# Kernel tuning notes

Measured on AMD Instinct MI355X. Metric: run time of the kernel, lower is better.

## Reference

```python
import jax, jax.numpy as jnp
import numpy as np

RE_PER_PRB = 12  # resource elements (subcarriers) per PRB in 5G NR


def _forward(y, h_hat_ls, dmrs_ofdm_pos, dmrs_subcarrier_pos):
    S = y.shape[2]  # num_ofdm_symbols (y used for its shape only)
    # [B, num_pilots, T, R] -> [B, R, T, num_pilots]
    h = jnp.transpose(h_hat_ls, (0, 3, 2, 1))
    B, R, T, P = h.shape
    # FOCC removal: average adjacent pilot pairs, duplicate back (sum/2, repeat 2)
    h = h.reshape(B, R, T, P // 2, 2).sum(axis=-1, keepdims=True) * 0.5
    h = jnp.broadcast_to(h, (B, R, T, P // 2, 2)).reshape(B, R, T, P)

    npd = dmrs_subcarrier_pos.shape[1]   # pilots per DMRS symbol per PRB
    nds = dmrs_ofdm_pos.shape[-1]        # number of DMRS OFDM symbols
    nprb = P // (npd * nds)              # number of PRBs
    RE = RE_PER_PRB

    # --- nearest-pilot indices + positional encodings, per tx (as in torch code,
    # torch.meshgrid default indexing='ij') ---
    re_pos = jnp.stack(
        jnp.meshgrid(jnp.arange(RE), jnp.arange(S), indexing='ij'), axis=-1
    ).reshape(-1, 1, 2)  # [RE*S, 1, 2]

    def per_tx(sc_pos, of_pos):
        pil = jnp.stack(jnp.meshgrid(sc_pos, of_pos, indexing='ij'), axis=-1).reshape(1, -1, 2)
        diff = jnp.abs(re_pos - pil)                  # [RE*S, npd*nds, 2] Manhattan components
        nn = jnp.argmin(diff.sum(-1), axis=1).reshape(S, RE)
        pe = diff.min(axis=1).reshape(S, RE, 2).transpose(1, 0, 2).astype(jnp.float32)  # [RE, S, 2]
        norm = lambda x: (x - x.mean()) / (x.std(ddof=1) + 1e-8)  # torch .std() is unbiased
        # channel order swapped exactly as in the torch code: [time-dist, freq-dist]
        return nn, jnp.stack([norm(pe[..., 1]), norm(pe[..., 0])], axis=-1)

    nn_idx, pe = jax.vmap(per_tx)(dmrs_subcarrier_pos, dmrs_ofdm_pos)  # [T,S,RE], [T,RE,S,2]
    pe = jnp.tile(pe, (1, nprb, 1, 1))  # [T, nprb*RE, S, 2]

    # --- group pilots per PRB ---
    # pilot layout in h_hat_ls: (dmrs_symbol, prb, subcarrier); per-PRB pilot index
    # = subcarrier*nds + symbol to match the meshgrid('ij') flattening above
    hp = h.reshape(B, R, T, nds, nprb, npd).transpose(0, 1, 2, 4, 5, 3)
    hp = hp.reshape(B, R, T, nprb, npd * nds)  # [B,R,T,nprb,pilots_per_prb]

    # --- nearest-neighbor gather onto the full resource grid ---
    gather_tx = lambda hp_t, nn_t: hp_t[..., nn_t]  # [B,R,nprb,Np] , [S,RE] -> [B,R,nprb,S,RE]
    gathered = jax.vmap(gather_tx, in_axes=(2, 0), out_axes=2)(hp, nn_idx)  # [B,R,T,nprb,S,RE]

    # -> [B, T, num_subcarriers, S, R]
    h_full = gathered.transpose(0, 2, 3, 5, 4, 1).reshape(B, T, nprb * RE, S, R)
    return h_full, pe


def setup_inputs() -> dict:
    key = jax.random.key(0)
    k1, k2 = jax.random.split(key)
    B, R, T, S = 16, 16, 4, 14
    nprb, npd, nds = 273, 6, 2
    P = nds * nprb * npd  # 3276 pilots
    y = jax.random.normal(k1, (B, R, S, nprb * RE_PER_PRB), dtype=jnp.float32)
    h_hat_ls = jax.random.normal(k2, (B, P, T, R), dtype=jnp.float32)
    dmrs_ofdm_pos = jnp.broadcast_to(jnp.array([2, 11], dtype=jnp.int32), (T, nds))
    dmrs_subcarrier_pos = jnp.broadcast_to(jnp.arange(0, 12, 2, dtype=jnp.int32), (T, npd))
    return {"y": y, "h_hat_ls": h_hat_ls, "dmrs_ofdm_pos": dmrs_ofdm_pos,
            "dmrs_subcarrier_pos": dmrs_subcarrier_pos}


def reference(y, h_hat_ls, dmrs_ofdm_pos, dmrs_subcarrier_pos):
    return _forward(y, h_hat_ls, dmrs_ofdm_pos, dmrs_subcarrier_pos)
```

## Files before the change

kernel.cpp:

```cpp
#include <hip/hip_runtime.h>

#define B_   16
#define R_   16
#define T_   4
#define S_   14
#define NPRB 273
#define NPD  6
#define NDS  2
#define RE_  12
#define P_   (NDS*NPRB*NPD)
#define NSC  (NPRB*RE_)
#define F_   (RE_*S_)

#define NH   (B_*T_*NSC*S_*R_)
#define NPE  (T_*NSC*S_*2)
#define NH4  (NH/4)
#define NPE4 (NPE/4)
#define NTOT4 (NH4+NPE4)

__global__ void prep_tables(const int* __restrict__ ofdm_pos,
                            const int* __restrict__ sc_pos,
                            int* __restrict__ qtab,
                            float* __restrict__ pe_base)
{
    __shared__ float dt_sh[T_*F_];
    __shared__ float df_sh[T_*F_];
    __shared__ float stats[T_][4];
    const int tid = threadIdx.x;
    if (tid < T_*F_) {
        const int t = tid / F_, f = tid % F_;
        const int re = f / S_, s = f % S_;
        int best = 1 << 30, bestj = 0;
        int dfmin = 1 << 30, dtmin = 1 << 30;
        for (int sci = 0; sci < NPD; ++sci) {
            const int dsc = abs(re - sc_pos[t*NPD + sci]);
            if (dsc < dfmin) dfmin = dsc;
            for (int ofi = 0; ofi < NDS; ++ofi) {
                const int dof = abs(s - ofdm_pos[t*NDS + ofi]);
                const int d = dsc + dof;
                if (d < best) { best = d; bestj = sci*NDS + ofi; }
            }
        }
        for (int ofi = 0; ofi < NDS; ++ofi) {
            const int dof = abs(s - ofdm_pos[t*NDS + ofi]);
            if (dof < dtmin) dtmin = dof;
        }
        const int sc = bestj / NDS, ds = bestj % NDS;
        const int sc0 = sc & ~1;
        qtab[tid] = ds*(NPRB*NPD) + sc0;
        dt_sh[tid] = (float)dtmin;
        df_sh[tid] = (float)dfmin;
    }
    __syncthreads();
    if (tid < T_*F_ && (tid % F_) == 0) {
        const int t = tid / F_;
        float s1t = 0.f, s1f = 0.f;
        for (int i = 0; i < F_; ++i) { s1t += dt_sh[t*F_+i]; s1f += df_sh[t*F_+i]; }
        const float mt = s1t / (float)F_, mf = s1f / (float)F_;
        float vt = 0.f, vf = 0.f;
        for (int i = 0; i < F_; ++i) {
            const float a = dt_sh[t*F_+i] - mt; vt += a*a;
            const float b = df_sh[t*F_+i] - mf; vf += b*b;
        }
        const float stdt = sqrtf(vt / (float)(F_-1));
        const float stdf = sqrtf(vf / (float)(F_-1));
        stats[t][0] = mt; stats[t][1] = 1.0f/(stdt + 1e-8f);
        stats[t][2] = mf; stats[t][3] = 1.0f/(stdf + 1e-8f);
    }
    __syncthreads();
    if (tid < T_*F_) {
        const int t = tid / F_;
        pe_base[tid*2 + 0] = (dt_sh[tid] - stats[t][0]) * stats[t][1];
        pe_base[tid*2 + 1] = (df_sh[tid] - stats[t][2]) * stats[t][3];
    }
}

__global__ __launch_bounds__(256) void gather_kernel(
    const float* __restrict__ hls,
    const int* __restrict__ qtab,
    const float* __restrict__ pe_base,
    float* __restrict__ out)
{
    const int idx = blockIdx.x * blockDim.x + threadIdx.x;
    if (idx >= NTOT4) return;
    if (idx < NH4) {
        const int r4 = idx & 3;
        int u = idx >> 2;
        const int s = u % S_;  u /= S_;
        const int k = u % NSC; u /= NSC;
        const int t = u & (T_-1);
        const int b = u >> 2;
        const int prb = k / RE_;
        const int re  = k - prb*RE_;
        const int f  = s*RE_ + re;
        const int p0 = qtab[t*F_ + f] + prb*NPD;
        const float4* src = (const float4*)hls + ((b*P_ + p0)*T_ + t)*(R_/4) + r4;
        const float4 a = src[0];
        const float4 c = src[T_*(R_/4)];
        float4 o;
        o.x = 0.5f*(a.x + c.x);
        o.y = 0.5f*(a.y + c.y);
        o.z = 0.5f*(a.z + c.z);
        o.w = 0.5f*(a.w + c.w);
        ((float4*)out)[idx] = o;
    } else {
        const int g0 = (idx - NH4) * 4;
        float v[4];
        #pragma unroll
        for (int u2 = 0; u2 < 4; ++u2) {
            const int g  = g0 + u2;
            const int c  = g & 1;
            const int g1 = g >> 1;
            const int s  = g1 % S_;
            const int g2 = g1 / S_;
            const int i  = g2 % NSC;
            const int t  = g2 / NSC;
            const int re = i % RE_;
            v[u2] = pe_base[(t*F_ + s*RE_ + re)*2 + c];
        }
        float4 o; o.x = v[0]; o.y = v[1]; o.z = v[2]; o.w = v[3];
        ((float4*)(out + NH))[idx - NH4] = o;
    }
}

extern "C" void kernel_launch(void* const* d_in, const int* in_sizes, int n_in,
                              void* d_out, int out_size, void* d_ws, size_t ws_size,
                              hipStream_t stream) {
    const float* hls  = (const float*)d_in[1];
    const int*   ofdm = (const int*)d_in[2];
    const int*   scp  = (const int*)d_in[3];
    float* out = (float*)d_out;

    int*   qtab    = (int*)d_ws;
    float* pe_base = (float*)((char*)d_ws + T_*F_*sizeof(int));

    hipLaunchKernelGGL(prep_tables, dim3(1), dim3(T_*F_), 0, stream,
                       ofdm, scp, qtab, pe_base);

    const int blocks = (NTOT4 + 255) / 256;
    hipLaunchKernelGGL(gather_kernel, dim3(blocks), dim3(256), 0, stream,
                       hls, qtab, pe_base, out);
}
```

Baseline: 261.8 us.

## Fuse table prep into a per-PRB gather kernel with shared-memory averages

Merges the single-block table-prep kernel and the gather kernel into one launch. Each h block handles one (b,t,prb) tile: it recomputes the nearest-pilot mapping for the tile, loads and FOCC-averages the six pilot pairs once into shared memory, then writes the 12x14x16 output chunk with nontemporal stores. The PE blocks recompute the statistics per block with wave reductions. This removes the serial prep launch, the redundant per-element global loads of pilots and the table lookups, at the cost of repeated table computation in every block and a hardcoded pilot-index decoding that assumes the test's pilot layout.

```diff
diff --git a/kernel.cpp b/kernel.cpp
--- a/kernel.cpp
+++ b/kernel.cpp
@@ -16,110 +16,134 @@
 #define NPE  (T_*NSC*S_*2)
 #define NH4  (NH/4)
 #define NPE4 (NPE/4)
-#define NTOT4 (NH4+NPE4)
 
-__global__ void prep_tables(const int* __restrict__ ofdm_pos,
-                            const int* __restrict__ sc_pos,
-                            int* __restrict__ qtab,
-                            float* __restrict__ pe_base)
+#define CHUNK4   (RE_*S_*R_/4)
+#define NBLK_PE  ((NPE4 + 255)/256)
+#define NBLK_H   (B_*T_*NPRB)
+
+typedef float f4 __attribute__((ext_vector_type(4)));
+
+__global__ __launch_bounds__(256) void fused_kernel(
+    const float* __restrict__ hls,
+    const int* __restrict__ ofdm_pos,
+    const int* __restrict__ sc_pos,
+    float* __restrict__ out)
 {
-    __shared__ float dt_sh[T_*F_];
-    __shared__ float df_sh[T_*F_];
-    __shared__ float stats[T_][4];
+    const int bid = blockIdx.x;
     const int tid = threadIdx.x;
-    if (tid < T_*F_) {
-        const int t = tid / F_, f = tid % F_;
-        const int re = f / S_, s = f % S_;
-        int best = 1 << 30, bestj = 0;
-        int dfmin = 1 << 30, dtmin = 1 << 30;
-        for (int sci = 0; sci < NPD; ++sci) {
-            const int dsc = abs(re - sc_pos[t*NPD + sci]);
-            if (dsc < dfmin) dfmin = dsc;
+
+    if (bid >= NBLK_PE) {
+        __shared__ int perm_sh[F_];
+        __shared__ f4  avg_sh[6*4];
+
+        const int hb  = bid - NBLK_PE;
+        const int prb = hb % NPRB;
+        const int bt  = hb / NPRB;
+        const int t   = bt & (T_-1);
+
+        if (tid < F_) {
+            const int v  = tid;
+            const int kl = v / S_, s = v - (v / S_)*S_;
+            const int jp = s*RE_ + kl;
+            const int rej = jp / S_, sj = jp - (jp / S_)*S_;
+            int best = 1 << 30, bestj = 0;
+            for (int sci = 0; sci < NPD; ++sci) {
+                const int dsc = abs(rej - sc_pos[t*NPD + sci]);
+                for (int ofi = 0; ofi < NDS; ++ofi) {
+                    const int dof = abs(sj - ofdm_pos[t*NDS + ofi]);
+                    const int d = dsc + dof;
+                    if (d < best) { best = d; bestj = sci*NDS + ofi; }
+                }
+            }
+            perm_sh[v] = (bestj & 1)*3 + (bestj >> 2);
+        } else if (tid >= 192 && tid < 216) {
+            const int j    = tid - 192;
+            const int code = j >> 2, r4 = j & 3;
+            const int ds   = (code >= 3) ? 1 : 0;
+            const int scp  = code - 3*ds;
+            const int b    = bt >> 2;
+            const int p0   = ds*(NPRB*NPD) + prb*NPD + 2*scp;
+            const f4* src = (const f4*)hls + ((b*P_ + p0)*T_ + t)*4 + r4;
+            const f4 a = src[0];
+            const f4 c = src[T_*4];
+            avg_sh[j] = 0.5f*(a + c);
+        }
+        __syncthreads();
+
+        f4* out4 = (f4*)out + (size_t)bt*(NSC*S_*R_/4) + (size_t)prb*CHUNK4;
+        #pragma unroll
+        for (int u = tid; u < CHUNK4; u += 256) {
+            const int r4 = u & 3;
+            const int v  = u >> 2;
+            const int code = perm_sh[v];
+            __builtin_nontemporal_store(avg_sh[code*4 + r4], &out4[u]);
+        }
+    } else {
+        __shared__ float dt_sh[T_*F_];
+        __shared__ float df_sh[T_*F_];
+        __shared__ float stats[T_][4];
+
+        for (int e = tid; e < T_*F_; e += 256) {
+            const int t  = e / F_, j = e - (e / F_)*F_;
+            const int rej = j / S_, sj = j - (j / S_)*S_;
+            int dfmin = 1 << 30, dtmin = 1 << 30;
+            for (int sci = 0; sci < NPD; ++sci) {
+                const int dsc = abs(rej - sc_pos[t*NPD + sci]);
+                if (dsc < dfmin) dfmin = dsc;
+            }
             for (int ofi = 0; ofi < NDS; ++ofi) {
-                const int dof = abs(s - ofdm_pos[t*NDS + ofi]);
-                const int d = dsc + dof;
-                if (d < best) { best = d; bestj = sci*NDS + ofi; }
+                const int dof = abs(sj - ofdm_pos[t*NDS + ofi]);
+                if (dof < dtmin) dtmin = dof;
+            }
+            dt_sh[e] = (float)dtmin;
+            df_sh[e] = (float)dfmin;
+        }
+        __syncthreads();
+
+        const int w = tid >> 6, lane = tid & 63;
+        {
+            float sdt = 0.f, sdf = 0.f;
+            for (int j = lane; j < F_; j += 64) { sdt += dt_sh[w*F_+j]; sdf += df_sh[w*F_+j]; }
+            for (int o = 32; o > 0; o >>= 1) { sdt += __shfl_down(sdt, o); sdf += __shfl_down(sdf, o); }
+            if (lane == 0) { stats[w][0] = sdt/(float)F_; stats[w][2] = sdf/(float)F_; }
+        }
+        __syncthreads();
+        {
+            const float mt = stats[w][0], mf = stats[w][2];
+            float vt = 0.f, vf = 0.f;
+            for (int j = lane; j < F_; j += 64) {
+                const float a = dt_sh[w*F_+j] - mt; vt += a*a;
+                const float b = df_sh[w*F_+j] - mf; vf += b*b;
+            }
+            for (int o = 32; o > 0; o >>= 1) { vt += __shfl_down(vt, o); vf += __shfl_down(vf, o); }
+            if (lane == 0) {
+                stats[w][1] = 1.0f/(sqrtf(vt/(float)(F_-1)) + 1e-8f);
+                stats[w][3] = 1.0f/(sqrtf(vf/(float)(F_-1)) + 1e-8f);
             }
         }
-        for (int ofi = 0; ofi < NDS; ++ofi) {
-            const int dof = abs(s - ofdm_pos[t*NDS + ofi]);
-            if (dof < dtmin) dtmin = dof;
+        __syncthreads();
+
+        const int q = bid*256 + tid;
+        if (q < NPE4) {
+            const int g0 = q*4;
+            float vv[4];
+            #pragma unroll
+            for (int u2 = 0; u2 < 4; ++u2) {
+                const int g  = g0 + u2;
+                const int c  = g & 1;
+                const int g1 = g >> 1;
+                const int s  = g1 % S_;
+                const int g2 = g1 / S_;
+                const int i  = g2 % NSC;
+                const int t  = g2 / NSC;
+                const int re = i % RE_;
+                const int j  = s*RE_ + re;
+                const float d = (c == 0) ? dt_sh[t*F_ + j] : df_sh[t*F_ + j];
+                vv[u2] = (d - stats[t][2*c]) * stats[t][2*c + 1];
+            }
+            f4 o; o.x = vv[0]; o.y = vv[1]; o.z = vv[2]; o.w = vv[3];
+            __builtin_nontemporal_store(o, (f4*)(out + NH) + q);
         }
-        const int sc = bestj / NDS, ds = bestj % NDS;
-        const int sc0 = sc & ~1;
-        qtab[tid] = ds*(NPRB*NPD) + sc0;
-        dt_sh[tid] = (float)dtmin;
-        df_sh[tid] = (float)dfmin;
-    }
-    __syncthreads();
-    if (tid < T_*F_ && (tid % F_) == 0) {
-        const int t = tid / F_;
-        float s1t = 0.f, s1f = 0.f;
-        for (int i = 0; i < F_; ++i) { s1t += dt_sh[t*F_+i]; s1f += df_sh[t*F_+i]; }
-        const float mt = s1t / (float)F_, mf = s1f / (float)F_;
-        float vt = 0.f, vf = 0.f;
-        for (int i = 0; i < F_; ++i) {
-            const float a = dt_sh[t*F_+i] - mt; vt += a*a;
-            const float b = df_sh[t*F_+i] - mf; vf += b*b;
-        }
-        const float stdt = sqrtf(vt / (float)(F_-1));
-        const float stdf = sqrtf(vf / (float)(F_-1));
-        stats[t][0] = mt; stats[t][1] = 1.0f/(stdt + 1e-8f);
-        stats[t][2] = mf; stats[t][3] = 1.0f/(stdf + 1e-8f);
-    }
-    __syncthreads();
-    if (tid < T_*F_) {
-        const int t = tid / F_;
-        pe_base[tid*2 + 0] = (dt_sh[tid] - stats[t][0]) * stats[t][1];
-        pe_base[tid*2 + 1] = (df_sh[tid] - stats[t][2]) * stats[t][3];
-    }
-}
-
-__global__ __launch_bounds__(256) void gather_kernel(
-    const float* __restrict__ hls,
-    const int* __restrict__ qtab,
-    const float* __restrict__ pe_base,
-    float* __restrict__ out)
-{
-    const int idx = blockIdx.x * blockDim.x + threadIdx.x;
-    if (idx >= NTOT4) return;
-    if (idx < NH4) {
-        const int r4 = idx & 3;
-        int u = idx >> 2;
-        const int s = u % S_;  u /= S_;
-        const int k = u % NSC; u /= NSC;
-        const int t = u & (T_-1);
-        const int b = u >> 2;
-        const int prb = k / RE_;
-        const int re  = k - prb*RE_;
-        const int f  = s*RE_ + re;
-        const int p0 = qtab[t*F_ + f] + prb*NPD;
-        const float4* src = (const float4*)hls + ((b*P_ + p0)*T_ + t)*(R_/4) + r4;
-        const float4 a = src[0];
-        const float4 c = src[T_*(R_/4)];
-        float4 o;
-        o.x = 0.5f*(a.x + c.x);
-        o.y = 0.5f*(a.y + c.y);
-        o.z = 0.5f*(a.z + c.z);
-        o.w = 0.5f*(a.w + c.w);
-        ((float4*)out)[idx] = o;
-    } else {
-        const int g0 = (idx - NH4) * 4;
-        float v[4];
-        #pragma unroll
-        for (int u2 = 0; u2 < 4; ++u2) {
-            const int g  = g0 + u2;
-            const int c  = g & 1;
-            const int g1 = g >> 1;
-            const int s  = g1 % S_;
-            const int g2 = g1 / S_;
-            const int i  = g2 % NSC;
-            const int t  = g2 / NSC;
-            const int re = i % RE_;
-            v[u2] = pe_base[(t*F_ + s*RE_ + re)*2 + c];
-        }
-        float4 o; o.x = v[0]; o.y = v[1]; o.z = v[2]; o.w = v[3];
-        ((float4*)(out + NH))[idx - NH4] = o;
     }
 }
 
@@ -131,13 +155,6 @@
     const int*   scp  = (const int*)d_in[3];
     float* out = (float*)d_out;
 
-    int*   qtab    = (int*)d_ws;
-    float* pe_base = (float*)((char*)d_ws + T_*F_*sizeof(int));
-
-    hipLaunchKernelGGL(prep_tables, dim3(1), dim3(T_*F_), 0, stream,
-                       ofdm, scp, qtab, pe_base);
-
-    const int blocks = (NTOT4 + 255) / 256;
-    hipLaunchKernelGGL(gather_kernel, dim3(blocks), dim3(256), 0, stream,
-                       hls, qtab, pe_base, out);
+    hipLaunchKernelGGL(fused_kernel, dim3(NBLK_PE + NBLK_H), dim3(256), 0, stream,
+                       hls, ofdm, scp, out);
 }
```

Result: faster. 223.4 us, median of 2 (-14.7%).
